# Kernel optimization log

Hardware: AMD Instinct MI355X
Metric: run time of the kernel (lower is better)

## Reference

```python
import jax, jax.numpy as jnp
import numpy as np

N_NODES = 100000
N_EDGES = 1600000
F_IN = 128
EMB = 128
N_GRAPHS = 128
G_FEAT = 32


def setup_inputs() -> dict:
    key = jax.random.key(0)
    ks = jax.random.split(key, 12)
    s = 0.02
    return {
        "x": jax.random.normal(ks[0], (N_NODES, F_IN), dtype=jnp.float32),
        "edges_idx": jax.random.randint(ks[1], (2, N_EDGES), 0, N_NODES),
        "batch_idx": jnp.sort(jax.random.randint(ks[2], (N_NODES,), 0, N_GRAPHS)),
        "g_features": jax.random.normal(ks[3], (N_GRAPHS, G_FEAT), dtype=jnp.float32),
        # SAGEConv 0: lin_l (aggregated neighbors, with bias), lin_r (root, no bias)
        "W_l0": jax.random.normal(ks[4], (F_IN, EMB), dtype=jnp.float32) * s,
        "b_l0": jnp.zeros((EMB,), dtype=jnp.float32),
        "W_r0": jax.random.normal(ks[5], (F_IN, EMB), dtype=jnp.float32) * s,
        # SAGEConv 1
        "W_l1": jax.random.normal(ks[6], (EMB, EMB), dtype=jnp.float32) * s,
        "b_l1": jnp.zeros((EMB,), dtype=jnp.float32),
        "W_r1": jax.random.normal(ks[7], (EMB, EMB), dtype=jnp.float32) * s,
        # lin_g
        "W_g": jax.random.normal(ks[8], (G_FEAT, EMB), dtype=jnp.float32) * s,
        "b_g": jnp.zeros((EMB,), dtype=jnp.float32),
        # out_layer: 3*emb -> 2 (mean pool | max pool | g features)
        "W_o": jax.random.normal(ks[9], (3 * EMB, 2), dtype=jnp.float32) * s,
        "b_o": jnp.zeros((2,), dtype=jnp.float32),
    }


def _sage_conv(x, src, tgt, W_l, b_l, W_r, n_nodes):
    # PyG SAGEConv with mean aggregation: out = lin_l(mean_j x_j) + lin_r(x_i)
    msg = x[src]                                                   # [E, d] gather
    agg = jax.ops.segment_sum(msg, tgt, num_segments=n_nodes)      # [N, d]
    cnt = jax.ops.segment_sum(jnp.ones((src.shape[0], 1), x.dtype), tgt,
                              num_segments=n_nodes)                # [N, 1]
    agg = agg / jnp.maximum(cnt, 1.0)
    return agg @ W_l + b_l + x @ W_r


def reference(x, edges_idx, batch_idx, g_features,
              W_l0, b_l0, W_r0, W_l1, b_l1, W_r1, W_g, b_g, W_o, b_o):
    src, tgt = edges_idx[0], edges_idx[1]
    n = x.shape[0]
    # layer 0 + relu (dropout is identity in eval mode)
    h = jax.nn.relu(_sage_conv(x, src, tgt, W_l0, b_l0, W_r0, n))
    # layer 1 (no activation) then readout
    h = _sage_conv(h, src, tgt, W_l1, b_l1, W_r1, n)
    # global mean / max pool over graphs
    g_sum = jax.ops.segment_sum(h, batch_idx, num_segments=N_GRAPHS)
    g_cnt = jax.ops.segment_sum(jnp.ones((n, 1), h.dtype), batch_idx,
                                num_segments=N_GRAPHS)
    g_mean = g_sum / jnp.maximum(g_cnt, 1.0)
    g_max = jax.ops.segment_max(h, batch_idx, num_segments=N_GRAPHS)
    flat = jnp.concatenate([g_mean, g_max, g_features @ W_g + b_g], axis=1)
    return jax.nn.log_softmax(flat @ W_o + b_o, axis=-1)
```

## Files before the change

### kernel.cpp

```cpp
#include <hip/hip_runtime.h>

#define N_NODES  100000
#define N_EDGESC 1600000
#define EMB      128
#define N_GRAPHS 128
#define G_FEAT   32

#define BUKSH    9
#define NBUK     196
#define CHUNK_E  2048
#define NBLK_E   ((N_EDGESC + CHUNK_E - 1) / CHUNK_E)

typedef __attribute__((ext_vector_type(8))) short bf16x8;
typedef __attribute__((ext_vector_type(4))) float f32x4;

__device__ __forceinline__ unsigned fkey(float f) {
  unsigned u = __float_as_uint(f);
  return (u & 0x80000000u) ? ~u : (u | 0x80000000u);
}
__device__ __forceinline__ float fkey_inv(unsigned k) {
  return (k & 0x80000000u) ? __uint_as_float(k & 0x7FFFFFFFu)
                           : __uint_as_float(~k);
}
__device__ __forceinline__ float bf2f(unsigned short u) {
  return __uint_as_float(((unsigned)u) << 16);
}
__device__ __forceinline__ unsigned short f2bf(float f) {
  unsigned u = __float_as_uint(f);
  u += 0x7fffu + ((u >> 16) & 1u);
  return (unsigned short)(u >> 16);
}


__global__ __launch_bounds__(256) void f2bf_kernel(const float* __restrict__ in,
                                                   unsigned short* __restrict__ out,
                                                   int n4) {
  int i = blockIdx.x * blockDim.x + threadIdx.x;
  if (i >= n4) return;
  float4 v = reinterpret_cast<const float4*>(in)[i];
  uint2 o;
  o.x = (unsigned)f2bf(v.x) | ((unsigned)f2bf(v.y) << 16);
  o.y = (unsigned)f2bf(v.z) | ((unsigned)f2bf(v.w) << 16);
  reinterpret_cast<uint2*>(out)[i] = o;
}

__global__ __launch_bounds__(256) void pack_kernel(const float* __restrict__ Wl,
                                                   const float* __restrict__ Wr,
                                                   unsigned short* __restrict__ pack) {
  int id = blockIdx.x * blockDim.x + threadIdx.x;
  if (id >= 4096) return;
  int lane = id & 63;
  int kb = (id >> 6) & 7;
  int cb = id >> 9;
  int col = cb * 16 + (lane & 15);
  int k0 = kb * 32 + (lane >> 4) * 8;
  unsigned short v[8];
#pragma unroll
  for (int j = 0; j < 8; j++) {
    int k = k0 + j;
    float w = (k < 128) ? Wl[k * 128 + col] : Wr[(k - 128) * 128 + col];
    v[j] = f2bf(w);
  }
  uint4 o;
  o.x = (unsigned)v[0] | ((unsigned)v[1] << 16);
  o.y = (unsigned)v[2] | ((unsigned)v[3] << 16);
  o.z = (unsigned)v[4] | ((unsigned)v[5] << 16);
  o.w = (unsigned)v[6] | ((unsigned)v[7] << 16);
  *reinterpret_cast<uint4*>(pack + (size_t)id * 8) = o;
}


__global__ __launch_bounds__(256) void bhistA_kernel(const int* __restrict__ tgti,
                                                     int* __restrict__ counts) {
  __shared__ int h[NBUK];
  for (int i = threadIdx.x; i < NBUK; i += 256) h[i] = 0;
  __syncthreads();
  int base = blockIdx.x * CHUNK_E;
  for (int i = threadIdx.x; i < CHUNK_E; i += 256) {
    int e = base + i;
    if (e < N_EDGESC) atomicAdd(&h[tgti[e] >> BUKSH], 1);
  }
  __syncthreads();
  for (int i = threadIdx.x; i < NBUK; i += 256)
    counts[blockIdx.x * NBUK + i] = h[i];
}

__global__ __launch_bounds__(256) void bsumB1_kernel(const int* __restrict__ counts,
                                                     int* __restrict__ tot) {
  __shared__ int sh[256];
  int b = blockIdx.x;
  int t = threadIdx.x;
  int s = 0;
  for (int blk = t; blk < NBLK_E; blk += 256) s += counts[blk * NBUK + b];
  sh[t] = s;
  __syncthreads();
  for (int off = 128; off > 0; off >>= 1) {
    if (t < off) sh[t] += sh[t + off];
    __syncthreads();
  }
  if (t == 0) tot[b] = sh[0];
}

__global__ __launch_bounds__(256) void bbaseB_kernel(const int* __restrict__ tot,
                                                     int* __restrict__ bucketBase) {
  __shared__ int sh[256];
  int t = threadIdx.x;
  int v = (t < NBUK) ? tot[t] : 0;
  sh[t] = v;
  __syncthreads();
  for (int off = 1; off < 256; off <<= 1) {
    int val = (t >= off) ? sh[t - off] : 0;
    __syncthreads();
    if (t >= off) sh[t] += val;
    __syncthreads();
  }
  if (t < NBUK) bucketBase[t] = sh[t] - v;
  if (t == 0) bucketBase[NBUK] = sh[NBUK - 1];
}

__global__ __launch_bounds__(256) void boffB2_kernel(const int* __restrict__ counts,
                                                     const int* __restrict__ bucketBase,
                                                     int* __restrict__ offsets) {
  __shared__ int sh[256];
  int b = blockIdx.x;
  int t = threadIdx.x;
  int v[4], s = 0;
#pragma unroll
  for (int i = 0; i < 4; i++) {
    int blk = t * 4 + i;
    v[i] = (blk < NBLK_E) ? counts[blk * NBUK + b] : 0;
    s += v[i];
  }
  sh[t] = s;
  __syncthreads();
  for (int off = 1; off < 256; off <<= 1) {
    int val = (t >= off) ? sh[t - off] : 0;
    __syncthreads();
    if (t >= off) sh[t] += val;
    __syncthreads();
  }
  int run = bucketBase[b] + sh[t] - s;
#pragma unroll
  for (int i = 0; i < 4; i++) {
    int blk = t * 4 + i;
    if (blk < NBLK_E) offsets[blk * NBUK + b] = run;
    run += v[i];
  }
}

__global__ __launch_bounds__(256) void bscatC_kernel(const int* __restrict__ srci,
                                                     const int* __restrict__ tgti,
                                                     const int* __restrict__ offsets,
                                                     unsigned* __restrict__ bucketed) {
  __shared__ int cur[NBUK];
  for (int i = threadIdx.x; i < NBUK; i += 256)
    cur[i] = offsets[blockIdx.x * NBUK + i];
  __syncthreads();
  int base = blockIdx.x * CHUNK_E;
  for (int i = threadIdx.x; i < CHUNK_E; i += 256) {
    int e = base + i;
    if (e < N_EDGESC) {
      int t = tgti[e];
      int bk = t >> BUKSH;
      int pos = atomicAdd(&cur[bk], 1);
      bucketed[pos] = (unsigned)srci[e] |
                      ((unsigned)(t & ((1 << BUKSH) - 1)) << 17);
    }
  }
}

__global__ __launch_bounds__(256) void bcsrD_kernel(const unsigned* __restrict__ bucketed,
                                                    const int* __restrict__ bucketBase,
                                                    int* __restrict__ rowstart,
                                                    int* __restrict__ ebuf) {
  __shared__ int deg[512];
  __shared__ int pre[512];
  __shared__ int sh2[256];
  int bk = blockIdx.x;
  int node0 = bk << BUKSH;
  int nn = min(512, N_NODES - node0);
  int beg = bucketBase[bk], end = bucketBase[bk + 1];
  for (int i = threadIdx.x; i < 512; i += 256) deg[i] = 0;
  __syncthreads();
  for (int j = beg + threadIdx.x; j < end; j += 256)
    atomicAdd(&deg[bucketed[j] >> 17], 1);
  __syncthreads();
  int t = threadIdx.x;
  int v0 = deg[2 * t], v1 = deg[2 * t + 1];
  sh2[t] = v0 + v1;
  __syncthreads();
  for (int off = 1; off < 256; off <<= 1) {
    int val = (t >= off) ? sh2[t - off] : 0;
    __syncthreads();
    if (t >= off) sh2[t] += val;
    __syncthreads();
  }
  int ex = sh2[t] - v0 - v1;
  pre[2 * t] = ex;
  pre[2 * t + 1] = ex + v0;
  __syncthreads();
  for (int i = threadIdx.x; i < nn; i += 256) rowstart[node0 + i] = beg + pre[i];
  if (bk == 0 && threadIdx.x == 0) rowstart[N_NODES] = N_EDGESC;
  for (int i = threadIdx.x; i < 512; i += 256) deg[i] = pre[i];
  __syncthreads();
  for (int j = beg + threadIdx.x; j < end; j += 256) {
    unsigned p = bucketed[j];
    int ln = p >> 17;
    int pos = atomicAdd(&deg[ln], 1);
    ebuf[beg + pos] = (int)(p & 0x1FFFFu);
  }
}

__global__ __launch_bounds__(256) void aggb_kernel(const unsigned short* __restrict__ featB,
                                                   const int* __restrict__ ebuf,
                                                   const int* __restrict__ rowstart,
                                                   unsigned short* __restrict__ aggB) {
  int wid = (blockIdx.x * 256 + threadIdx.x) >> 6;
  int lane = threadIdx.x & 63;
  int node = wid * 2 + (lane >> 5);
  if (node >= N_NODES) return;
  int l = lane & 31;
  int beg = rowstart[node], end = rowstart[node + 1];
  const unsigned short* fb = featB + l * 4;
  float a0 = 0.0f, a1 = 0.0f, a2 = 0.0f, a3 = 0.0f;
  for (int j = beg; j < end; j += 8) {
    int idx[8];
    uint2 u[8];
#pragma unroll
    for (int i = 0; i < 8; i++) idx[i] = min(j + i, end - 1);
#pragma unroll
    for (int i = 0; i < 8; i++)
      u[i] = *reinterpret_cast<const uint2*>(fb + (size_t)ebuf[idx[i]] * EMB);
#pragma unroll
    for (int i = 0; i < 8; i++) {
      bool ok = (j + i) < end;
      unsigned ux = ok ? u[i].x : 0u;
      unsigned uy = ok ? u[i].y : 0u;
      a0 += bf2f((unsigned short)(ux & 0xffffu));
      a1 += bf2f((unsigned short)(ux >> 16));
      a2 += bf2f((unsigned short)(uy & 0xffffu));
      a3 += bf2f((unsigned short)(uy >> 16));
    }
  }
  float inv = 1.0f / fmaxf((float)(end - beg), 1.0f);
  uint2 o;
  o.x = (unsigned)f2bf(a0 * inv) | ((unsigned)f2bf(a1 * inv) << 16);
  o.y = (unsigned)f2bf(a2 * inv) | ((unsigned)f2bf(a3 * inv) << 16);
  *reinterpret_cast<uint2*>(aggB + (size_t)node * EMB + l * 4) = o;
}

template <bool RELU, bool POOL>
__global__ __launch_bounds__(256) void nodeMM_kernel(
    const unsigned short* __restrict__ aggB, const unsigned short* __restrict__ xB,
    const unsigned short* __restrict__ pack, const float* __restrict__ bl,
    const int* __restrict__ batch, unsigned short* __restrict__ hout,
    float* __restrict__ gsum, unsigned* __restrict__ gmax) {
  int w = threadIdx.x >> 6;
  int lane = threadIdx.x & 63;
  int wbase = blockIdx.x * 64 + w * 16;
  bool active = (wbase < N_NODES);

  f32x4 acc[8];
  if (active) {
    bf16x8 afrag[8];
    int row = wbase + (lane & 15);
    int koff = (lane >> 4) * 8;
    const unsigned short* ap = aggB + (size_t)row * EMB + koff;
    const unsigned short* xp = xB + (size_t)row * EMB + koff;
#pragma unroll
    for (int kb = 0; kb < 4; kb++) afrag[kb] = *reinterpret_cast<const bf16x8*>(ap + kb * 32);
#pragma unroll
    for (int kb = 0; kb < 4; kb++) afrag[4 + kb] = *reinterpret_cast<const bf16x8*>(xp + kb * 32);
#pragma unroll
    for (int cb = 0; cb < 8; cb++) {
      f32x4 a = {0.0f, 0.0f, 0.0f, 0.0f};
#pragma unroll
      for (int kb = 0; kb < 8; kb++) {
        bf16x8 b = *reinterpret_cast<const bf16x8*>(pack + ((size_t)(cb * 8 + kb) * 64 + lane) * 8);
        a = __builtin_amdgcn_mfma_f32_16x16x32_bf16(afrag[kb], b, a, 0, 0, 0);
      }
      acc[cb] = a;
    }
  }

  if constexpr (!POOL) {
    if (active) {
#pragma unroll
      for (int cb = 0; cb < 8; cb++) {
        int col = cb * 16 + (lane & 15);
        float bias = bl[col];
#pragma unroll
        for (int r = 0; r < 4; r++) {
          float v = acc[cb][r] + bias;
          if (RELU) v = fmaxf(v, 0.0f);
          int rowl = (lane >> 4) * 4 + r;
          hout[(size_t)(wbase + rowl) * EMB + col] = f2bf(v);
        }
      }
    }
  } else {
    __shared__ float sh[64][130];
    __shared__ int sBatch[64];
    if (threadIdx.x < 64) {
      int node = blockIdx.x * 64 + threadIdx.x;
      sBatch[threadIdx.x] = batch[node < N_NODES ? node : (N_NODES - 1)];
    }
    if (active) {
#pragma unroll
      for (int cb = 0; cb < 8; cb++) {
        int col = cb * 16 + (lane & 15);
        float bias = bl[col];
#pragma unroll
        for (int r = 0; r < 4; r++) {
          float v = acc[cb][r] + bias;
          if (RELU) v = fmaxf(v, 0.0f);
          sh[w * 16 + (lane >> 4) * 4 + r][col] = v;
        }
      }
    }
    __syncthreads();
    int col = threadIdx.x & 127;
    int half = threadIdx.x >> 7;
    int nbase = blockIdx.x * 64 + half * 32;
    float rs = 0.0f, rm = -INFINITY;
    int cur = -1;
    for (int r = 0; r < 32; r++) {
      if (nbase + r >= N_NODES) break;
      int b = sBatch[half * 32 + r];
      float v = sh[half * 32 + r][col];
      if (b != cur) {
        if (cur >= 0) {
          atomicAdd(&gsum[cur * EMB + col], rs);
          atomicMax(&gmax[cur * EMB + col], fkey(rm));
        }
        cur = b; rs = 0.0f; rm = -INFINITY;
      }
      rs += v;
      rm = fmaxf(rm, v);
    }
    if (cur >= 0) {
      atomicAdd(&gsum[cur * EMB + col], rs);
      atomicMax(&gmax[cur * EMB + col], fkey(rm));
    }
  }
}

__global__ __launch_bounds__(128) void gcnt_kernel(const int* __restrict__ batch,
                                                   float* __restrict__ gcnt) {
  __shared__ int lb[129];
  int g = threadIdx.x;
  int lo = 0, hi = N_NODES;
  while (lo < hi) {
    int mid = (lo + hi) >> 1;
    if (batch[mid] < g) lo = mid + 1; else hi = mid;
  }
  lb[g] = lo;
  if (g == 0) lb[128] = N_NODES;
  __syncthreads();
  gcnt[g] = (float)(lb[g + 1] - lb[g]);
}

__global__ __launch_bounds__(128) void readout_kernel(
    const float* __restrict__ gsum, const unsigned* __restrict__ gmax,
    const float* __restrict__ gcnt, const float* __restrict__ gfeat,
    const float* __restrict__ Wg, const float* __restrict__ bg,
    const float* __restrict__ Wo, const float* __restrict__ bo,
    float* __restrict__ out) {
  int g = blockIdx.x, d = threadIdx.x;
  float mean = gsum[g * EMB + d] / fmaxf(gcnt[g], 1.0f);
  float mx = fkey_inv(gmax[g * EMB + d]);
  float gfe = bg[d];
#pragma unroll
  for (int k = 0; k < G_FEAT; k++) gfe += gfeat[g * G_FEAT + k] * Wg[k * EMB + d];
  float l0 = mean * Wo[d * 2 + 0] + mx * Wo[(EMB + d) * 2 + 0] +
             gfe * Wo[(2 * EMB + d) * 2 + 0];
  float l1 = mean * Wo[d * 2 + 1] + mx * Wo[(EMB + d) * 2 + 1] +
             gfe * Wo[(2 * EMB + d) * 2 + 1];
  __shared__ float s0[128], s1[128];
  s0[d] = l0; s1[d] = l1;
  __syncthreads();
  for (int off = 64; off > 0; off >>= 1) {
    if (d < off) { s0[d] += s0[d + off]; s1[d] += s1[d + off]; }
    __syncthreads();
  }
  if (d == 0) {
    float a = s0[0] + bo[0];
    float b = s1[0] + bo[1];
    float m = fmaxf(a, b);
    float lse = m + logf(expf(a - m) + expf(b - m));
    out[g * 2 + 0] = a - lse;
    out[g * 2 + 1] = b - lse;
  }
}

extern "C" void kernel_launch(void* const* d_in, const int* in_sizes, int n_in,
                              void* d_out, int out_size, void* d_ws,
                              size_t ws_size, hipStream_t stream) {
  const float* x     = (const float*)d_in[0];
  const int*   edges = (const int*)d_in[1];
  const int*   batch = (const int*)d_in[2];
  const float* gfeat = (const float*)d_in[3];
  const float* W_l0  = (const float*)d_in[4];
  const float* b_l0  = (const float*)d_in[5];
  const float* W_r0  = (const float*)d_in[6];
  const float* W_l1  = (const float*)d_in[7];
  const float* b_l1  = (const float*)d_in[8];
  const float* W_r1  = (const float*)d_in[9];
  const float* W_g   = (const float*)d_in[10];
  const float* b_g   = (const float*)d_in[11];
  const float* W_o   = (const float*)d_in[12];
  const float* b_o   = (const float*)d_in[13];
  const int* srci = edges;
  const int* tgti = edges + N_EDGESC;

  char* ws = (char*)d_ws;
  float*    gsum     = (float*)ws;
  unsigned* gmax     = (unsigned*)(gsum + N_GRAPHS * EMB);
  float*    gcnt     = (float*)(gmax + N_GRAPHS * EMB);
  unsigned short* xB   = (unsigned short*)(gcnt + N_GRAPHS);
  unsigned short* aggB = xB + (size_t)N_NODES * EMB;
  unsigned short* hB   = aggB + (size_t)N_NODES * EMB;
  unsigned short* pack0 = hB + (size_t)N_NODES * EMB;
  unsigned short* pack1 = pack0 + 8 * 8 * 64 * 8;
  int*      ebuf     = (int*)(pack1 + 8 * 8 * 64 * 8);
  int*      rowstart = ebuf + N_EDGESC;
  int*      bucketBase = rowstart + N_NODES + 1;
  int*      tot      = bucketBase + NBUK + 4;
  int*      counts   = (int*)aggB;
  int*      offsets  = counts + NBLK_E * NBUK;
  unsigned* bucketed = (unsigned*)hB;

  size_t zbytes = (size_t)((char*)xB - ws);
  hipMemsetAsync(d_ws, 0, zbytes, stream);

  dim3 b256(256);

  f2bf_kernel<<<(N_NODES * EMB / 4 + 255) / 256, b256, 0, stream>>>(x, xB,
                                                                    N_NODES * EMB / 4);
  pack_kernel<<<16, b256, 0, stream>>>(W_l0, W_r0, pack0);
  pack_kernel<<<16, b256, 0, stream>>>(W_l1, W_r1, pack1);

  bhistA_kernel<<<NBLK_E, b256, 0, stream>>>(tgti, counts);
  bsumB1_kernel<<<NBUK, b256, 0, stream>>>(counts, tot);
  bbaseB_kernel<<<1, b256, 0, stream>>>(tot, bucketBase);
  boffB2_kernel<<<NBUK, b256, 0, stream>>>(counts, bucketBase, offsets);
  bscatC_kernel<<<NBLK_E, b256, 0, stream>>>(srci, tgti, offsets, bucketed);
  bcsrD_kernel<<<NBUK, b256, 0, stream>>>(bucketed, bucketBase, rowstart, ebuf);
  gcnt_kernel<<<1, 128, 0, stream>>>(batch, gcnt);

  int ngrid = (N_NODES + 63) / 64;
  int agrid = (N_NODES + 7) / 8;

  aggb_kernel<<<agrid, b256, 0, stream>>>(xB, ebuf, rowstart, aggB);
  nodeMM_kernel<true, false><<<ngrid, b256, 0, stream>>>(
      aggB, xB, pack0, b_l0, nullptr, hB, nullptr, nullptr);

  aggb_kernel<<<agrid, b256, 0, stream>>>(hB, ebuf, rowstart, aggB);
  nodeMM_kernel<false, true><<<ngrid, b256, 0, stream>>>(
      aggB, hB, pack1, b_l1, batch, nullptr, gsum, gmax);

  readout_kernel<<<N_GRAPHS, 128, 0, stream>>>(gsum, gmax, gcnt, gfeat, W_g,
                                               b_g, W_o, b_o, (float*)d_out);
}
```

Baseline: 353.8 us.

## Pad CSR rows to multiples of eight with a zero sentinel node

The CSR build now pads each node's neighbour list to a multiple of 8 entries. Padding slots point to a sentinel row N_NODES, which is zeroed in both feature buffers, and the per-node degree is stored separately. The aggregation loop can therefore drop the clamp and select logic and gather eight rows unconditionally, with bf16 unpacking simplified to shifts and masks. The cost is extra padded gathers that read the zero row, and a larger edge buffer with per-bucket slack.

```diff
diff --git a/kernel.cpp b/kernel.cpp
--- a/kernel.cpp
+++ b/kernel.cpp
@@ -10,6 +10,7 @@
 #define NBUK     196
 #define CHUNK_E  2048
 #define NBLK_E   ((N_EDGESC + CHUNK_E - 1) / CHUNK_E)
+#define PADSLK   4096
 
 typedef __attribute__((ext_vector_type(8))) short bf16x8;
 typedef __attribute__((ext_vector_type(4))) float f32x4;
@@ -21,9 +22,6 @@
 __device__ __forceinline__ float fkey_inv(unsigned k) {
   return (k & 0x80000000u) ? __uint_as_float(k & 0x7FFFFFFFu)
                            : __uint_as_float(~k);
-}
-__device__ __forceinline__ float bf2f(unsigned short u) {
-  return __uint_as_float(((unsigned)u) << 16);
 }
 __device__ __forceinline__ unsigned short f2bf(float f) {
   unsigned u = __float_as_uint(f);
@@ -172,22 +170,26 @@
 __global__ __launch_bounds__(256) void bcsrD_kernel(const unsigned* __restrict__ bucketed,
                                                     const int* __restrict__ bucketBase,
                                                     int* __restrict__ rowstart,
+                                                    int* __restrict__ degv,
                                                     int* __restrict__ ebuf) {
-  __shared__ int deg[512];
-  __shared__ int pre[512];
+  __shared__ int sdeg[512];
+  __shared__ int spre[512];
+  __shared__ int scur[512];
   __shared__ int sh2[256];
   int bk = blockIdx.x;
   int node0 = bk << BUKSH;
   int nn = min(512, N_NODES - node0);
   int beg = bucketBase[bk], end = bucketBase[bk + 1];
-  for (int i = threadIdx.x; i < 512; i += 256) deg[i] = 0;
+  int padBase = beg + bk * PADSLK;
+  for (int i = threadIdx.x; i < 512; i += 256) sdeg[i] = 0;
   __syncthreads();
   for (int j = beg + threadIdx.x; j < end; j += 256)
-    atomicAdd(&deg[bucketed[j] >> 17], 1);
+    atomicAdd(&sdeg[bucketed[j] >> 17], 1);
   __syncthreads();
   int t = threadIdx.x;
-  int v0 = deg[2 * t], v1 = deg[2 * t + 1];
-  sh2[t] = v0 + v1;
+  int d0 = sdeg[2 * t], d1 = sdeg[2 * t + 1];
+  int p0 = (d0 + 7) & ~7, p1 = (d1 + 7) & ~7;
+  sh2[t] = p0 + p1;
   __syncthreads();
   for (int off = 1; off < 256; off <<= 1) {
     int val = (t >= off) ? sh2[t - off] : 0;
@@ -195,57 +197,63 @@
     if (t >= off) sh2[t] += val;
     __syncthreads();
   }
-  int ex = sh2[t] - v0 - v1;
-  pre[2 * t] = ex;
-  pre[2 * t + 1] = ex + v0;
-  __syncthreads();
-  for (int i = threadIdx.x; i < nn; i += 256) rowstart[node0 + i] = beg + pre[i];
-  if (bk == 0 && threadIdx.x == 0) rowstart[N_NODES] = N_EDGESC;
-  for (int i = threadIdx.x; i < 512; i += 256) deg[i] = pre[i];
-  __syncthreads();
-  for (int j = beg + threadIdx.x; j < end; j += 256) {
+  int ex = sh2[t] - p0 - p1;
+  spre[2 * t] = ex;
+  spre[2 * t + 1] = ex + p0;
+  __syncthreads();
+  for (int i = t; i < nn; i += 256) {
+    rowstart[node0 + i] = padBase + spre[i];
+    degv[node0 + i] = sdeg[i];
+  }
+  for (int i = t; i < 512; i += 256) scur[i] = spre[i];
+  __syncthreads();
+  for (int j = beg + t; j < end; j += 256) {
     unsigned p = bucketed[j];
     int ln = p >> 17;
-    int pos = atomicAdd(&deg[ln], 1);
-    ebuf[beg + pos] = (int)(p & 0x1FFFFu);
+    int pos = atomicAdd(&scur[ln], 1);
+    ebuf[padBase + pos] = (int)(p & 0x1FFFFu);
+  }
+  for (int i = t; i < nn; i += 256) {
+    int d = sdeg[i];
+    int dp = (d + 7) & ~7;
+    for (int p = d; p < dp; p++) ebuf[padBase + spre[i] + p] = N_NODES;
   }
 }
 
 __global__ __launch_bounds__(256) void aggb_kernel(const unsigned short* __restrict__ featB,
                                                    const int* __restrict__ ebuf,
                                                    const int* __restrict__ rowstart,
+                                                   const int* __restrict__ degv,
                                                    unsigned short* __restrict__ aggB) {
   int wid = (blockIdx.x * 256 + threadIdx.x) >> 6;
   int lane = threadIdx.x & 63;
   int node = wid * 2 + (lane >> 5);
   if (node >= N_NODES) return;
   int l = lane & 31;
-  int beg = rowstart[node], end = rowstart[node + 1];
+  int beg = rowstart[node];
+  int d = degv[node];
+  int endp = beg + ((d + 7) & ~7);
   const unsigned short* fb = featB + l * 4;
-  float a0 = 0.0f, a1 = 0.0f, a2 = 0.0f, a3 = 0.0f;
-  for (int j = beg; j < end; j += 8) {
-    int idx[8];
+  float2 A0 = {0.0f, 0.0f}, A1 = {0.0f, 0.0f};
+  for (int j = beg; j < endp; j += 8) {
     uint2 u[8];
 #pragma unroll
-    for (int i = 0; i < 8; i++) idx[i] = min(j + i, end - 1);
-#pragma unroll
-    for (int i = 0; i < 8; i++)
-      u[i] = *reinterpret_cast<const uint2*>(fb + (size_t)ebuf[idx[i]] * EMB);
-#pragma unroll
     for (int i = 0; i < 8; i++) {
-      bool ok = (j + i) < end;
-      unsigned ux = ok ? u[i].x : 0u;
-      unsigned uy = ok ? u[i].y : 0u;
-      a0 += bf2f((unsigned short)(ux & 0xffffu));
-      a1 += bf2f((unsigned short)(ux >> 16));
-      a2 += bf2f((unsigned short)(uy & 0xffffu));
-      a3 += bf2f((unsigned short)(uy >> 16));
-    }
-  }
-  float inv = 1.0f / fmaxf((float)(end - beg), 1.0f);
+      int s = ebuf[j + i];
+      u[i] = *reinterpret_cast<const uint2*>(fb + (size_t)s * EMB);
+    }
+#pragma unroll
+    for (int i = 0; i < 8; i++) {
+      A0.x += __uint_as_float(u[i].x << 16);
+      A0.y += __uint_as_float(u[i].x & 0xffff0000u);
+      A1.x += __uint_as_float(u[i].y << 16);
+      A1.y += __uint_as_float(u[i].y & 0xffff0000u);
+    }
+  }
+  float inv = 1.0f / fmaxf((float)d, 1.0f);
   uint2 o;
-  o.x = (unsigned)f2bf(a0 * inv) | ((unsigned)f2bf(a1 * inv) << 16);
-  o.y = (unsigned)f2bf(a2 * inv) | ((unsigned)f2bf(a3 * inv) << 16);
+  o.x = (unsigned)f2bf(A0.x * inv) | ((unsigned)f2bf(A0.y * inv) << 16);
+  o.y = (unsigned)f2bf(A1.x * inv) | ((unsigned)f2bf(A1.y * inv) << 16);
   *reinterpret_cast<uint2*>(aggB + (size_t)node * EMB + l * 4) = o;
 }
 
@@ -418,13 +426,14 @@
   unsigned* gmax     = (unsigned*)(gsum + N_GRAPHS * EMB);
   float*    gcnt     = (float*)(gmax + N_GRAPHS * EMB);
   unsigned short* xB   = (unsigned short*)(gcnt + N_GRAPHS);
-  unsigned short* aggB = xB + (size_t)N_NODES * EMB;
+  unsigned short* aggB = xB + (size_t)(N_NODES + 1) * EMB;
   unsigned short* hB   = aggB + (size_t)N_NODES * EMB;
-  unsigned short* pack0 = hB + (size_t)N_NODES * EMB;
+  unsigned short* pack0 = hB + (size_t)(N_NODES + 1) * EMB;
   unsigned short* pack1 = pack0 + 8 * 8 * 64 * 8;
   int*      ebuf     = (int*)(pack1 + 8 * 8 * 64 * 8);
-  int*      rowstart = ebuf + N_EDGESC;
-  int*      bucketBase = rowstart + N_NODES + 1;
+  int*      rowstart = ebuf + N_EDGESC + NBUK * PADSLK;
+  int*      degv     = rowstart + N_NODES + 1;
+  int*      bucketBase = degv + N_NODES;
   int*      tot      = bucketBase + NBUK + 4;
   int*      counts   = (int*)aggB;
   int*      offsets  = counts + NBLK_E * NBUK;
@@ -432,6 +441,8 @@
 
   size_t zbytes = (size_t)((char*)xB - ws);
   hipMemsetAsync(d_ws, 0, zbytes, stream);
+  hipMemsetAsync(xB + (size_t)N_NODES * EMB, 0, EMB * sizeof(unsigned short), stream);
+  hipMemsetAsync(hB + (size_t)N_NODES * EMB, 0, EMB * sizeof(unsigned short), stream);
 
   dim3 b256(256);
 
@@ -445,17 +456,17 @@
   bbaseB_kernel<<<1, b256, 0, stream>>>(tot, bucketBase);
   boffB2_kernel<<<NBUK, b256, 0, stream>>>(counts, bucketBase, offsets);
   bscatC_kernel<<<NBLK_E, b256, 0, stream>>>(srci, tgti, offsets, bucketed);
-  bcsrD_kernel<<<NBUK, b256, 0, stream>>>(bucketed, bucketBase, rowstart, ebuf);
+  bcsrD_kernel<<<NBUK, b256, 0, stream>>>(bucketed, bucketBase, rowstart, degv, ebuf);
   gcnt_kernel<<<1, 128, 0, stream>>>(batch, gcnt);
 
   int ngrid = (N_NODES + 63) / 64;
   int agrid = (N_NODES + 7) / 8;
 
-  aggb_kernel<<<agrid, b256, 0, stream>>>(xB, ebuf, rowstart, aggB);
+  aggb_kernel<<<agrid, b256, 0, stream>>>(xB, ebuf, rowstart, degv, aggB);
   nodeMM_kernel<true, false><<<ngrid, b256, 0, stream>>>(
       aggB, xB, pack0, b_l0, nullptr, hB, nullptr, nullptr);
 
-  aggb_kernel<<<agrid, b256, 0, stream>>>(hB, ebuf, rowstart, aggB);
+  aggb_kernel<<<agrid, b256, 0, stream>>>(hB, ebuf, rowstart, degv, aggB);
   nodeMM_kernel<false, true><<<ngrid, b256, 0, stream>>>(
       aggB, hB, pack1, b_l1, batch, nullptr, gsum, gmax);
 
```

After: 363.2 us. +2.7%, slower.
